# Kernel tuning notes

Measured on AMD Instinct MI355X. Metric: run time of the kernel, lower is better.

## Reference

```python
import jax, jax.numpy as jnp
import numpy as np

B, F, DIN, HID, H, E, NC = 2048, 32, 64, 128, 4, 262144, 10
N = B * F  # 65536 nodes


def setup_inputs() -> dict:
    key = jax.random.key(0)
    ks = jax.random.split(key, 20)
    p = lambda k, shape: jax.random.normal(k, shape, jnp.float32) * 0.05
    return {
        "emb": jax.random.normal(ks[0], (B, F, DIN), jnp.float32),
        "edge_index": jax.random.randint(ks[1], (2, E), 0, N, jnp.int32),
        "batch": (jnp.arange(N, dtype=jnp.int32) // F),
        # aligner Linear(64 -> 128)
        "W_align": p(ks[2], (DIN, HID)), "b_align": p(ks[3], (HID,)),
        # GATConv1: 128 -> 128, heads=4, concat
        "W1": p(ks[4], (HID, H * HID)),
        "att_src1": p(ks[5], (H, HID)), "att_dst1": p(ks[6], (H, HID)),
        "b1": p(ks[7], (H * HID,)),
        # GATConv2: 512 -> 128, heads=1, concat=False
        "W2": p(ks[8], (H * HID, HID)),
        "att_src2": p(ks[9], (1, HID)), "att_dst2": p(ks[10], (1, HID)),
        "b2": p(ks[11], (HID,)),
        # classifier MLP 128 -> 64 -> 10
        "Wc1": p(ks[12], (HID, HID // 2)), "bc1": p(ks[13], (HID // 2,)),
        "Wc2": p(ks[14], (HID // 2, NC)), "bc2": p(ks[15], (NC,)),
    }


def _gat(x, src, dst, W, a_src, a_dst, b, concat):
    # PyG GATConv (eval mode): per-edge additive attention + segment softmax over dst.
    n = x.shape[0]
    h, c = a_src.shape
    hx = (x @ W).reshape(n, h, c)                       # [N,H,C]
    al_s = jnp.einsum('nhc,hc->nh', hx, a_src)          # [N,H]
    al_d = jnp.einsum('nhc,hc->nh', hx, a_dst)
    e = jax.nn.leaky_relu(al_s[src] + al_d[dst], 0.2)   # [E,H]
    m = jax.ops.segment_max(e, dst, num_segments=n)
    m = jnp.where(jnp.isfinite(m), m, 0.0)
    ex = jnp.exp(e - m[dst])
    denom = jax.ops.segment_sum(ex, dst, num_segments=n)
    alpha = ex / (denom[dst] + 1e-16)                   # [E,H]
    out = jax.ops.segment_sum(alpha[:, :, None] * hx[src], dst, num_segments=n)
    out = out.reshape(n, h * c) if concat else out.mean(axis=1)
    return out + b


def reference(emb, edge_index, batch, W_align, b_align, W1, att_src1, att_dst1, b1,
              W2, att_src2, att_dst2, b2, Wc1, bc1, Wc2, bc2):
    # fused align: Linear over stacked field embeddings, then flatten to nodes
    x = (emb @ W_align + b_align).reshape(N, HID)
    # add self-loops (PyG GATConv default)
    loop = jnp.arange(N, dtype=edge_index.dtype)
    src = jnp.concatenate([edge_index[0], loop])
    dst = jnp.concatenate([edge_index[1], loop])
    x = _gat(x, src, dst, W1, att_src1, att_dst1, b1, concat=True)
    x = jax.nn.elu(x)
    x = _gat(x, src, dst, W2, att_src2, att_dst2, b2, concat=False)
    # global mean pool per graph
    g = jax.ops.segment_sum(x, batch, num_segments=B)
    cnt = jax.ops.segment_sum(jnp.ones((N, 1), x.dtype), batch, num_segments=B)
    g = g / jnp.maximum(cnt, 1.0)
    # classifier head (dropout off in eval)
    hcls = jax.nn.leaky_relu(g @ Wc1 + bc1, 0.01)
    return hcls @ Wc2 + bc2
```

## Files before the change

### kernel.cpp

```cpp
#include <hip/hip_runtime.h>


namespace {

constexpr int NNODE = 65536;
constexpr int NEDGE = 262144;
constexpr int NGRAPH = 2048;
constexpr int FPG = 32;

typedef __attribute__((ext_vector_type(8))) short bf16x8;
typedef __attribute__((ext_vector_type(4))) float f32x4;

__device__ __forceinline__ float lrelu02(float x) { return x > 0.f ? x : 0.2f * x; }
__device__ __forceinline__ float bf_lo(unsigned u) { return __uint_as_float(u << 16); }
__device__ __forceinline__ float bf_hi(unsigned u) { return __uint_as_float(u & 0xffff0000u); }
__device__ __forceinline__ float b2f(unsigned short u) { return __uint_as_float(((unsigned)u) << 16); }
__device__ __forceinline__ unsigned short f2b(float f) {
  unsigned u = __float_as_uint(f);
  return (unsigned short)((u + 0x7fffu + ((u >> 16) & 1u)) >> 16);
}

__device__ __forceinline__ void gload16(const void* g, unsigned short* l) {
  __builtin_amdgcn_global_load_lds((const __attribute__((address_space(1))) void*)g,
                                   (__attribute__((address_space(3))) void*)l, 16, 0, 0);
}


__global__ __launch_bounds__(256) void prep_kernel(const float* __restrict__ W1, const float* __restrict__ W2,
                                                   const float* __restrict__ Wa, const float* __restrict__ as1,
                                                   const float* __restrict__ ad1, unsigned short* __restrict__ w1t,
                                                   unsigned short* __restrict__ w2t, unsigned short* __restrict__ wat,
                                                   float* __restrict__ vs1, float* __restrict__ vd1,
                                                   int* __restrict__ deg) {
  int b = blockIdx.x;
  int tid = threadIdx.x;
  if (b < 256) {
    int idx = b * 256 + tid;
    int n = idx >> 7, k = idx & 127;
    w1t[idx] = f2b(W1[(size_t)k * 512 + n]);
  } else if (b < 512) {
    int idx = (b - 256) * 256 + tid;
    int n = idx >> 9, k = idx & 511;
    w2t[idx] = f2b(W2[(size_t)k * 128 + n]);
  } else if (b < 544) {
    int idx = (b - 512) * 256 + tid;
    int n = idx >> 6, k = idx & 63;
    wat[idx] = f2b(Wa[(size_t)k * 128 + n]);
  } else if (b < 546) {
    int idx = (b - 544) * 256 + tid;
    int h = idx >> 7, c = idx & 127;
    float s = 0.f, d = 0.f;
    const float* wrow = W1 + (size_t)c * 512 + h * 128;
    const float* ar = as1 + h * 128;
    const float* dr = ad1 + h * 128;
    for (int j = 0; j < 128; ++j) {
      float w = wrow[j];
      s += w * ar[j];
      d += w * dr[j];
    }
    vs1[idx] = s;
    vd1[idx] = d;
  } else {
    int idx = (b - 546) * 256 + tid;
    int4 z;
    z.x = 0; z.y = 0; z.z = 0; z.w = 0;
    *(int4*)&deg[idx * 4] = z;
  }
}


__global__ __launch_bounds__(256) void hist_kernel(const int* __restrict__ dst, int* __restrict__ deg) {
  int e = blockIdx.x * 256 + threadIdx.x;
  if (e < NEDGE) atomicAdd(&deg[dst[e]], 1);
}

__global__ __launch_bounds__(1024) void scan_kernel(const int* __restrict__ deg, int* __restrict__ rowptr,
                                                    int* __restrict__ cursor) {
  __shared__ int sums[1024];
  int t = threadIdx.x;
  int base = t * 64;
  int d[64];
  int s = 0;
#pragma unroll
  for (int i = 0; i < 16; ++i) {
    int4 v = *(const int4*)&deg[base + i * 4];
    d[4 * i] = v.x; d[4 * i + 1] = v.y; d[4 * i + 2] = v.z; d[4 * i + 3] = v.w;
    s += v.x + v.y + v.z + v.w;
  }
  sums[t] = s;
  __syncthreads();
  for (int off = 1; off < 1024; off <<= 1) {
    int v = (t >= off) ? sums[t - off] : 0;
    __syncthreads();
    sums[t] += v;
    __syncthreads();
  }
  int run = (t == 0) ? 0 : sums[t - 1];
#pragma unroll
  for (int i = 0; i < 16; ++i) {
    int4 r;
    r.x = run; run += d[4 * i];
    r.y = run; run += d[4 * i + 1];
    r.z = run; run += d[4 * i + 2];
    r.w = run; run += d[4 * i + 3];
    *(int4*)&rowptr[base + i * 4] = r;
    *(int4*)&cursor[base + i * 4] = r;
  }
  if (t == 1023) rowptr[NNODE] = run;
}

__global__ __launch_bounds__(256) void scatter_kernel(const int* __restrict__ src, const int* __restrict__ dst,
                                                      int* __restrict__ cursor, int* __restrict__ csr_src,
                                                      int* __restrict__ csr_dst) {
  int e = blockIdx.x * 256 + threadIdx.x;
  if (e < NEDGE) {
    int s = src[e], d = dst[e];
    int p = atomicAdd(&cursor[d], 1);
    csr_src[p] = s;
    csr_dst[p] = d;
  }
}


__global__ __launch_bounds__(256) void edgew1_kernel(const int* __restrict__ csr_src, const int* __restrict__ csr_dst,
                                                     const float* __restrict__ al_s, const float* __restrict__ al_d,
                                                     float* __restrict__ w1) {
  int p = blockIdx.x * 256 + threadIdx.x;
  if (p >= NEDGE) return;
  int s = csr_src[p], d = csr_dst[p];
  float4 as = *(const float4*)&al_s[s * 4];
  float4 ad = *(const float4*)&al_d[d * 4];
  float4 w;
  w.x = expf(lrelu02(as.x + ad.x));
  w.y = expf(lrelu02(as.y + ad.y));
  w.z = expf(lrelu02(as.z + ad.z));
  w.w = expf(lrelu02(as.w + ad.w));
  *(float4*)&w1[(size_t)p * 4] = w;
}

__global__ __launch_bounds__(256) void edgew2_kernel(const int* __restrict__ csr_src, const int* __restrict__ csr_dst,
                                                     const float* __restrict__ al_s, const float* __restrict__ al_d,
                                                     float* __restrict__ w2) {
  int p = blockIdx.x * 256 + threadIdx.x;
  if (p >= NEDGE) return;
  w2[p] = expf(lrelu02(al_s[csr_src[p]] + al_d[csr_dst[p]]));
}


__device__ __forceinline__ bf16x8 frag_ld(const unsigned short* lds, int row, int kbyte) {
  const char* base = (const char*)lds + row * 128;
  int sw = (row & 7) << 4;
  uint2 lo = *(const uint2*)(base + (kbyte ^ sw));
  uint2 hi = *(const uint2*)(base + ((kbyte + 32) ^ sw));
  union { bf16x8 v; uint2 u2[2]; } f;
  f.u2[0] = lo;
  f.u2[1] = hi;
  return f.v;
}

__device__ __forceinline__ bf16x8 frag_ld_x(const unsigned short* lds, int row, int kbyte) {
  const char* base = (const char*)lds + row * 256;
  int sw = (row & 7) << 4;
  uint2 lo = *(const uint2*)(base + (kbyte ^ sw));
  uint2 hi = *(const uint2*)(base + ((kbyte + 32) ^ sw));
  union { bf16x8 v; uint2 u2[2]; } f;
  f.u2[0] = lo;
  f.u2[1] = hi;
  return f.v;
}


__global__ __launch_bounds__(256) void align_mfma_kernel(const float* __restrict__ emb,
                                                         const unsigned short* __restrict__ wat,
                                                         const float* __restrict__ bias,
                                                         unsigned short* __restrict__ x0) {
  __shared__ char smem[36864];
  unsigned short* Ae = (unsigned short*)smem;
  unsigned short* Wt = (unsigned short*)(smem + 16384);
  const int tid = threadIdx.x;
  const int lane = tid & 63;
  const int w = tid >> 6;
  const size_t bm = (size_t)blockIdx.x * 128;
  const int ln = lane & 15, lg = lane >> 4;
  const int kb0 = lg << 3;

  {
    int r8 = lane >> 3;
    int b8 = (lane & 7) << 4;
#pragma unroll
    for (int i = 0; i < 4; ++i) {
      int row = w * 32 + i * 8 + r8;
      int bcol = b8 ^ ((row & 7) << 4);
      gload16((const char*)wat + row * 128 + bcol, Wt + w * 2048 + i * 512);
    }
  }
#pragma unroll
  for (int i = 0; i < 4; ++i) {
    int slot = i * 256 + tid;
    int row = slot >> 3;
    int c16 = slot & 7;
    const float* sp = emb + (bm + row) * 64 + c16 * 8;
    float4 a = *(const float4*)sp;
    float4 b = *(const float4*)(sp + 4);
    ushort4 o0, o1;
    o0.x = f2b(a.x); o0.y = f2b(a.y); o0.z = f2b(a.z); o0.w = f2b(a.w);
    o1.x = f2b(b.x); o1.y = f2b(b.y); o1.z = f2b(b.z); o1.w = f2b(b.w);
    char* dp = (char*)Ae + row * 128 + ((c16 * 16) ^ ((row & 7) << 4));
    *(ushort4*)dp = o0;
    *(ushort4*)(dp + 8) = o1;
  }
  __syncthreads();

  f32x4 zero = {0.f, 0.f, 0.f, 0.f};
  f32x4 acc[2][8];
#pragma unroll
  for (int i = 0; i < 2; ++i)
#pragma unroll
    for (int j = 0; j < 8; ++j) acc[i][j] = zero;

#pragma unroll
  for (int kw = 0; kw < 2; ++kw) {
    bf16x8 af0 = frag_ld(Ae, w * 32 + ln, kw * 64 + kb0);
    bf16x8 af1 = frag_ld(Ae, w * 32 + 16 + ln, kw * 64 + kb0);
#pragma unroll
    for (int nf = 0; nf < 8; ++nf) {
      bf16x8 bfr = frag_ld(Wt, nf * 16 + ln, kw * 64 + kb0);
      acc[0][nf] = __builtin_amdgcn_mfma_f32_16x16x32_bf16(af0, bfr, acc[0][nf], 0, 0, 0);
      acc[1][nf] = __builtin_amdgcn_mfma_f32_16x16x32_bf16(af1, bfr, acc[1][nf], 0, 0, 0);
    }
  }

  float bval[8];
#pragma unroll
  for (int nf = 0; nf < 8; ++nf) bval[nf] = bias[nf * 16 + ln];
  __syncthreads();
  unsigned short* Cs = (unsigned short*)smem;
#pragma unroll
  for (int mf = 0; mf < 2; ++mf) {
#pragma unroll
    for (int r = 0; r < 4; ++r) {
      unsigned short* rp = Cs + (w * 32 + mf * 16 + lg * 4 + r) * 136 + ln;
#pragma unroll
      for (int nf = 0; nf < 8; ++nf) rp[nf * 16] = f2b(acc[mf][nf][r] + bval[nf]);
    }
  }
  __syncthreads();
  const int r16 = tid >> 4;
  const int cchunk = (tid & 15) * 8;
#pragma unroll
  for (int it = 0; it < 8; ++it) {
    int row = it * 16 + r16;
    *(uint4*)(x0 + (bm + row) * 128 + cchunk) = *(const uint4*)(Cs + row * 136 + cchunk);
  }
}


__global__ __launch_bounds__(256, 2) void fused12_kernel(const unsigned short* __restrict__ ybar,
                                                         const unsigned short* __restrict__ w1t,
                                                         const unsigned short* __restrict__ w2t,
                                                         const float* __restrict__ b1,
                                                         unsigned short* __restrict__ hx2) {
  __shared__ char smem[65536];
  unsigned short* Ws = (unsigned short*)smem;
  unsigned short* Ys = Ws + 16384;

  const int tid = threadIdx.x;
  const int lane = tid & 63;
  const int w = tid >> 6;
  const size_t bm = (size_t)blockIdx.x * 128;

  const int ln = lane & 15, lg = lane >> 4;
  const int kb0 = lg << 3;
  const int drow = lane >> 4;
  const int dcol = (lane & 15) << 4;

  f32x4 zero = {0.f, 0.f, 0.f, 0.f};
  f32x4 acc2[2][8];
#pragma unroll
  for (int i = 0; i < 2; ++i)
#pragma unroll
    for (int j = 0; j < 8; ++j) acc2[i][j] = zero;

  for (int h = 0; h < 4; ++h) {
    if (h) __syncthreads();
#pragma unroll
    for (int i = 0; i < 8; ++i) {
      int row = w * 32 + i * 4 + drow;
      int bcol = dcol ^ ((row & 7) << 4);
      gload16((const char*)w1t + ((size_t)(h * 128 + row) << 8) + bcol, Ws + w * 4096 + i * 512);
      gload16((const char*)ybar + ((bm + row) << 10) + (h << 8) + bcol, Ys + w * 4096 + i * 512);
    }
    __syncthreads();

    f32x4 acc1[8][2];
#pragma unroll
    for (int i = 0; i < 8; ++i) {
      acc1[i][0] = zero;
      acc1[i][1] = zero;
    }
#pragma unroll
    for (int kw = 0; kw < 4; ++kw) {
      bf16x8 bfr0 = frag_ld_x(Ys, w * 32 + ln, kw * 64 + kb0);
      bf16x8 bfr1 = frag_ld_x(Ys, w * 32 + 16 + ln, kw * 64 + kb0);
#pragma unroll
      for (int ct = 0; ct < 8; ++ct) {
        bf16x8 af = frag_ld_x(Ws, ct * 16 + ln, kw * 64 + kb0);
        acc1[ct][0] = __builtin_amdgcn_mfma_f32_16x16x32_bf16(af, bfr0, acc1[ct][0], 0, 0, 0);
        acc1[ct][1] = __builtin_amdgcn_mfma_f32_16x16x32_bf16(af, bfr1, acc1[ct][1], 0, 0, 0);
      }
    }
    __syncthreads();

#pragma unroll
    for (int i = 0; i < 8; ++i) {
      int row = w * 32 + i * 4 + drow;
      int bcol = dcol ^ ((row & 7) << 4);
      gload16((const char*)w2t + ((size_t)row << 10) + (h << 8) + bcol, Ws + w * 4096 + i * 512);
    }
    __syncthreads();

#pragma unroll
    for (int kw = 0; kw < 4; ++kw) {
      float4 b_lo = *(const float4*)&b1[h * 128 + kw * 32 + lg * 4];
      float4 b_hi = *(const float4*)&b1[h * 128 + kw * 32 + 16 + lg * 4];
      bf16x8 af2[2];
#pragma unroll
      for (int mf = 0; mf < 2; ++mf) {
        union { bf16x8 v; unsigned short u[8]; } t;
#pragma unroll
        for (int r = 0; r < 4; ++r) {
          float vlo = acc1[2 * kw][mf][r] + ((const float*)&b_lo)[r];
          float vhi = acc1[2 * kw + 1][mf][r] + ((const float*)&b_hi)[r];
          vlo = vlo > 0.f ? vlo : __expf(vlo) - 1.f;
          vhi = vhi > 0.f ? vhi : __expf(vhi) - 1.f;
          t.u[r] = f2b(vlo);
          t.u[4 + r] = f2b(vhi);
        }
        af2[mf] = t.v;
      }
#pragma unroll
      for (int nf = 0; nf < 8; ++nf) {
        bf16x8 bfr = frag_ld_x(Ws, nf * 16 + ln, kw * 64 + kb0);
        acc2[0][nf] = __builtin_amdgcn_mfma_f32_16x16x32_bf16(af2[0], bfr, acc2[0][nf], 0, 0, 0);
        acc2[1][nf] = __builtin_amdgcn_mfma_f32_16x16x32_bf16(af2[1], bfr, acc2[1][nf], 0, 0, 0);
      }
    }
  }

  __syncthreads();
  unsigned short* Cs = (unsigned short*)smem;
#pragma unroll
  for (int mf = 0; mf < 2; ++mf) {
#pragma unroll
    for (int r = 0; r < 4; ++r) {
      unsigned short* rp = Cs + (w * 32 + mf * 16 + lg * 4 + r) * 136 + ln;
#pragma unroll
      for (int nf = 0; nf < 8; ++nf) rp[nf * 16] = f2b(acc2[mf][nf][r]);
    }
  }
  __syncthreads();
  const int r16 = tid >> 4;
  const int cchunk = (tid & 15) * 8;
#pragma unroll
  for (int it = 0; it < 8; ++it) {
    int row = it * 16 + r16;
    *(uint4*)(hx2 + (bm + row) * 128 + cchunk) = *(const uint4*)(Cs + row * 136 + cchunk);
  }
}


__global__ __launch_bounds__(256) void al1_kernel(const unsigned short* __restrict__ x0,
                                                  const float* __restrict__ vs1, const float* __restrict__ vd1,
                                                  float* __restrict__ al_s, float* __restrict__ al_d) {
  int n = blockIdx.x * 4 + (threadIdx.x >> 6);
  int lane = threadIdx.x & 63;
  unsigned v = *(const unsigned*)&x0[(size_t)n * 128 + lane * 2];
  float v0 = bf_lo(v), v1 = bf_hi(v);
  float r[8];
#pragma unroll
  for (int h = 0; h < 4; ++h) {
    float2 as = *(const float2*)&vs1[h * 128 + lane * 2];
    float2 ad = *(const float2*)&vd1[h * 128 + lane * 2];
    r[h] = v0 * as.x + v1 * as.y;
    r[4 + h] = v0 * ad.x + v1 * ad.y;
  }
#pragma unroll
  for (int off = 32; off; off >>= 1) {
#pragma unroll
    for (int j = 0; j < 8; ++j) r[j] += __shfl_xor(r[j], off);
  }
  if (lane < 4)
    al_s[n * 4 + lane] = r[lane];
  else if (lane < 8)
    al_d[n * 4 + lane - 4] = r[lane];
}

__global__ __launch_bounds__(256) void al2_kernel(const unsigned short* __restrict__ hx,
                                                  const float* __restrict__ att_src,
                                                  const float* __restrict__ att_dst,
                                                  float* __restrict__ al_s, float* __restrict__ al_d) {
  int n = blockIdx.x * 4 + (threadIdx.x >> 6);
  int lane = threadIdx.x & 63;
  unsigned v = *(const unsigned*)&hx[(size_t)n * 128 + lane * 2];
  float v0 = bf_lo(v), v1 = bf_hi(v);
  float2 as = *(const float2*)&att_src[lane * 2];
  float2 ad = *(const float2*)&att_dst[lane * 2];
  float s = v0 * as.x + v1 * as.y;
  float d = v0 * ad.x + v1 * ad.y;
  for (int off = 32; off; off >>= 1) {
    s += __shfl_down(s, off);
    d += __shfl_down(d, off);
  }
  if (lane == 0) {
    al_s[n] = s;
    al_d[n] = d;
  }
}


__global__ __launch_bounds__(256) void agg1_kernel(const unsigned short* __restrict__ x0,
                                                   const float* __restrict__ al_s, const float* __restrict__ al_d,
                                                   const int* __restrict__ rowptr, const int* __restrict__ csr_src,
                                                   const float* __restrict__ w1, unsigned short* __restrict__ ybar) {
  int n = blockIdx.x * 4 + (threadIdx.x >> 6);
  int c2 = (threadIdx.x & 63) * 2;
  float4 As4 = *(const float4*)&al_s[n * 4];
  float4 Ad4 = *(const float4*)&al_d[n * 4];
  float w00 = expf(lrelu02(As4.x + Ad4.x));
  float w01 = expf(lrelu02(As4.y + Ad4.y));
  float w02 = expf(lrelu02(As4.z + Ad4.z));
  float w03 = expf(lrelu02(As4.w + Ad4.w));
  unsigned u = *(const unsigned*)&x0[(size_t)n * 128 + c2];
  float lo = bf_lo(u), hi = bf_hi(u);
  float a00 = w00 * lo, a01 = w01 * lo, a02 = w02 * lo, a03 = w03 * lo;
  float a10 = w00 * hi, a11 = w01 * hi, a12 = w02 * hi, a13 = w03 * hi;
  float d0 = w00, d1 = w01, d2 = w02, d3 = w03;
  int p0 = rowptr[n], p1 = rowptr[n + 1];
  int p = p0;
  for (; p + 4 <= p1; p += 4) {
    int s0 = csr_src[p], s1 = csr_src[p + 1], s2 = csr_src[p + 2], s3 = csr_src[p + 3];
    float4 wA = *(const float4*)&w1[(size_t)p * 4];
    float4 wB = *(const float4*)&w1[(size_t)(p + 1) * 4];
    float4 wC = *(const float4*)&w1[(size_t)(p + 2) * 4];
    float4 wD = *(const float4*)&w1[(size_t)(p + 3) * 4];
    unsigned u0 = *(const unsigned*)&x0[(size_t)s0 * 128 + c2];
    unsigned u1 = *(const unsigned*)&x0[(size_t)s1 * 128 + c2];
    unsigned u2 = *(const unsigned*)&x0[(size_t)s2 * 128 + c2];
    unsigned u3 = *(const unsigned*)&x0[(size_t)s3 * 128 + c2];
    float l0 = bf_lo(u0), h0 = bf_hi(u0);
    float l1 = bf_lo(u1), h1 = bf_hi(u1);
    float l2 = bf_lo(u2), h2 = bf_hi(u2);
    float l3 = bf_lo(u3), h3 = bf_hi(u3);
    a00 += wA.x * l0 + wB.x * l1 + wC.x * l2 + wD.x * l3;
    a01 += wA.y * l0 + wB.y * l1 + wC.y * l2 + wD.y * l3;
    a02 += wA.z * l0 + wB.z * l1 + wC.z * l2 + wD.z * l3;
    a03 += wA.w * l0 + wB.w * l1 + wC.w * l2 + wD.w * l3;
    a10 += wA.x * h0 + wB.x * h1 + wC.x * h2 + wD.x * h3;
    a11 += wA.y * h0 + wB.y * h1 + wC.y * h2 + wD.y * h3;
    a12 += wA.z * h0 + wB.z * h1 + wC.z * h2 + wD.z * h3;
    a13 += wA.w * h0 + wB.w * h1 + wC.w * h2 + wD.w * h3;
    d0 += wA.x + wB.x + wC.x + wD.x;
    d1 += wA.y + wB.y + wC.y + wD.y;
    d2 += wA.z + wB.z + wC.z + wD.z;
    d3 += wA.w + wB.w + wC.w + wD.w;
  }
  for (; p < p1; ++p) {
    int s = csr_src[p];
    float4 wA = *(const float4*)&w1[(size_t)p * 4];
    unsigned uu = *(const unsigned*)&x0[(size_t)s * 128 + c2];
    float l = bf_lo(uu), hh = bf_hi(uu);
    a00 += wA.x * l; a01 += wA.y * l; a02 += wA.z * l; a03 += wA.w * l;
    a10 += wA.x * hh; a11 += wA.y * hh; a12 += wA.z * hh; a13 += wA.w * hh;
    d0 += wA.x; d1 += wA.y; d2 += wA.z; d3 += wA.w;
  }
  unsigned short* yb = ybar + (size_t)n * 512 + c2;
  float i0 = 1.f / (d0 + 1e-16f), i1 = 1.f / (d1 + 1e-16f);
  float i2 = 1.f / (d2 + 1e-16f), i3 = 1.f / (d3 + 1e-16f);
  ushort2 o;
  o.x = f2b(a00 * i0); o.y = f2b(a10 * i0); *(ushort2*)(yb + 0) = o;
  o.x = f2b(a01 * i1); o.y = f2b(a11 * i1); *(ushort2*)(yb + 128) = o;
  o.x = f2b(a02 * i2); o.y = f2b(a12 * i2); *(ushort2*)(yb + 256) = o;
  o.x = f2b(a03 * i3); o.y = f2b(a13 * i3); *(ushort2*)(yb + 384) = o;
}


__global__ __launch_bounds__(256) void agg2_kernel(const unsigned short* __restrict__ hx,
                                                   const float* __restrict__ al_s, const float* __restrict__ al_d,
                                                   const int* __restrict__ rowptr, const int* __restrict__ csr_src,
                                                   const float* __restrict__ w2, const float* __restrict__ b2,
                                                   unsigned short* __restrict__ out) {
  int n = blockIdx.x * 4 + (threadIdx.x >> 6);
  int c2 = (threadIdx.x & 63) * 2;
  float w0 = expf(lrelu02(al_s[n] + al_d[n]));
  unsigned u = *(const unsigned*)&hx[(size_t)n * 128 + c2];
  float acc0 = w0 * bf_lo(u), acc1 = w0 * bf_hi(u);
  float den = w0;
  int p0 = rowptr[n], p1 = rowptr[n + 1];
  int p = p0;
  for (; p + 4 <= p1; p += 4) {
    int s0 = csr_src[p], s1 = csr_src[p + 1], s2 = csr_src[p + 2], s3 = csr_src[p + 3];
    float wa = w2[p], wb = w2[p + 1], wc = w2[p + 2], wd = w2[p + 3];
    unsigned u0 = *(const unsigned*)&hx[(size_t)s0 * 128 + c2];
    unsigned u1 = *(const unsigned*)&hx[(size_t)s1 * 128 + c2];
    unsigned u2 = *(const unsigned*)&hx[(size_t)s2 * 128 + c2];
    unsigned u3 = *(const unsigned*)&hx[(size_t)s3 * 128 + c2];
    acc0 += wa * bf_lo(u0) + wb * bf_lo(u1) + wc * bf_lo(u2) + wd * bf_lo(u3);
    acc1 += wa * bf_hi(u0) + wb * bf_hi(u1) + wc * bf_hi(u2) + wd * bf_hi(u3);
    den += wa + wb + wc + wd;
  }
  for (; p < p1; ++p) {
    int s = csr_src[p];
    float w = w2[p];
    unsigned uu = *(const unsigned*)&hx[(size_t)s * 128 + c2];
    acc0 += w * bf_lo(uu);
    acc1 += w * bf_hi(uu);
    den += w;
  }
  float inv = 1.f / (den + 1e-16f);
  ushort2 o;
  o.x = f2b(acc0 * inv + b2[c2]);
  o.y = f2b(acc1 * inv + b2[c2 + 1]);
  *(ushort2*)&out[(size_t)n * 128 + c2] = o;
}


__global__ __launch_bounds__(128) void poolcls_kernel(const unsigned short* __restrict__ x,
                                                      const float* __restrict__ Wc1, const float* __restrict__ bc1,
                                                      const float* __restrict__ Wc2, const float* __restrict__ bc2,
                                                      float* __restrict__ out) {
  __shared__ float g[128];
  __shared__ float hcls[64];
  int b = blockIdx.x;
  int t = threadIdx.x;
  const unsigned short* base = x + (size_t)b * FPG * 128;
  float s = 0.f;
#pragma unroll
  for (int i = 0; i < FPG; ++i) s += b2f(base[i * 128 + t]);
  g[t] = s * (1.0f / FPG);
  __syncthreads();
  if (t < 64) {
    float a = bc1[t];
#pragma unroll 4
    for (int k = 0; k < 128; ++k) a += g[k] * Wc1[k * 64 + t];
    hcls[t] = a > 0.f ? a : 0.01f * a;
  }
  __syncthreads();
  if (t < 10) {
    float a = bc2[t];
#pragma unroll
    for (int k = 0; k < 64; ++k) a += hcls[k] * Wc2[k * 10 + t];
    out[b * 10 + t] = a;
  }
}

}

extern "C" void kernel_launch(void* const* d_in, const int* in_sizes, int n_in,
                              void* d_out, int out_size, void* d_ws, size_t ws_size,
                              hipStream_t stream) {
  const float* emb = (const float*)d_in[0];
  const int* edge = (const int*)d_in[1];
  const float* W_align = (const float*)d_in[3];
  const float* b_align = (const float*)d_in[4];
  const float* W1 = (const float*)d_in[5];
  const float* att_src1 = (const float*)d_in[6];
  const float* att_dst1 = (const float*)d_in[7];
  const float* b1 = (const float*)d_in[8];
  const float* W2 = (const float*)d_in[9];
  const float* att_src2 = (const float*)d_in[10];
  const float* att_dst2 = (const float*)d_in[11];
  const float* b2 = (const float*)d_in[12];
  const float* Wc1 = (const float*)d_in[13];
  const float* bc1 = (const float*)d_in[14];
  const float* Wc2 = (const float*)d_in[15];
  const float* bc2 = (const float*)d_in[16];

  char* ws = (char*)d_ws;
  size_t off = 0;
  auto alloc = [&](size_t bytes) -> char* {
    char* p = ws + off;
    off += (bytes + 255) & ~(size_t)255;
    return p;
  };
  unsigned short* x0 = (unsigned short*)alloc((size_t)NNODE * 128 * 2);
  unsigned short* ybar = (unsigned short*)alloc((size_t)NNODE * 512 * 2);
  unsigned short* hx2 = (unsigned short*)alloc((size_t)NNODE * 128 * 2);
  unsigned short* out2 = (unsigned short*)alloc((size_t)NNODE * 128 * 2);
  float* al_s1 = (float*)alloc((size_t)NNODE * 4 * 4);
  float* al_d1 = (float*)alloc((size_t)NNODE * 4 * 4);
  float* al_s2 = (float*)alloc((size_t)NNODE * 4);
  float* al_d2 = (float*)alloc((size_t)NNODE * 4);
  int* deg = (int*)alloc((size_t)NNODE * 4);
  int* rowptr = (int*)alloc((size_t)(NNODE + 1) * 4);
  int* cursor = (int*)alloc((size_t)NNODE * 4);
  int* csr_src = (int*)alloc((size_t)NEDGE * 4);
  int* csr_dst = (int*)alloc((size_t)NEDGE * 4);
  float* w1 = (float*)alloc((size_t)NEDGE * 4 * 4);
  float* w2 = (float*)alloc((size_t)NEDGE * 4);
  unsigned short* w1t = (unsigned short*)alloc((size_t)512 * 128 * 2);
  unsigned short* w2t = (unsigned short*)alloc((size_t)128 * 512 * 2);
  unsigned short* wat = (unsigned short*)alloc((size_t)128 * 64 * 2);
  float* vs1 = (float*)alloc((size_t)512 * 4);
  float* vd1 = (float*)alloc((size_t)512 * 4);

  const int* src = edge;
  const int* dst = edge + NEDGE;

  prep_kernel<<<610, 256, 0, stream>>>(W1, W2, W_align, att_src1, att_dst1,
                                       w1t, w2t, wat, vs1, vd1, deg);
  hist_kernel<<<NEDGE / 256, 256, 0, stream>>>(dst, deg);
  scan_kernel<<<1, 1024, 0, stream>>>(deg, rowptr, cursor);
  scatter_kernel<<<NEDGE / 256, 256, 0, stream>>>(src, dst, cursor, csr_src, csr_dst);

  align_mfma_kernel<<<512, 256, 0, stream>>>(emb, wat, b_align, x0);
  al1_kernel<<<NNODE / 4, 256, 0, stream>>>(x0, vs1, vd1, al_s1, al_d1);
  edgew1_kernel<<<NEDGE / 256, 256, 0, stream>>>(csr_src, csr_dst, al_s1, al_d1, w1);
  agg1_kernel<<<NNODE / 4, 256, 0, stream>>>(x0, al_s1, al_d1, rowptr, csr_src, w1, ybar);
  fused12_kernel<<<512, 256, 0, stream>>>(ybar, w1t, w2t, b1, hx2);
  al2_kernel<<<NNODE / 4, 256, 0, stream>>>(hx2, att_src2, att_dst2, al_s2, al_d2);
  edgew2_kernel<<<NEDGE / 256, 256, 0, stream>>>(csr_src, csr_dst, al_s2, al_d2, w2);
  agg2_kernel<<<NNODE / 4, 256, 0, stream>>>(hx2, al_s2, al_d2, rowptr, csr_src, w2, b2, out2);
  poolcls_kernel<<<NGRAPH, 128, 0, stream>>>(out2, Wc1, bc1, Wc2, bc2, (float*)d_out);
}
```

Measured before the change: 234.9 us.

## Load GAT weights directly from global and fuse layer-2 attention logits

The fused GEMM kernel no longer stages W1/W2 tiles in LDS. It reads weight fragments straight from global memory (relying on L2/cache) and keeps only a per-wave ybar tile in LDS, which removes most block-wide barriers and cuts shared memory to about 34KB, allowing more blocks per CU. The layer-2 attention dot products (al_s2/al_d2) are computed from the output tile already in LDS, so the separate al2 kernel launch and its re-read of hx2 are gone. The trade-off is uncoalesced, repeated global weight loads inside the MFMA loops, plus a serial 128-element dot product done by half the threads.

New measurement: 315.9 us. 1.34x slower.

```diff
diff --git a/kernel.cpp b/kernel.cpp
--- a/kernel.cpp
+++ b/kernel.cpp
@@ -158,14 +158,19 @@
   return f.v;
 }
 
-__device__ __forceinline__ bf16x8 frag_ld_x(const unsigned short* lds, int row, int kbyte) {
-  const char* base = (const char*)lds + row * 256;
+__device__ __forceinline__ bf16x8 ys_frag(const char* base, int row, int kbyte) {
+  const char* rb = base + row * 256;
   int sw = (row & 7) << 4;
-  uint2 lo = *(const uint2*)(base + (kbyte ^ sw));
-  uint2 hi = *(const uint2*)(base + ((kbyte + 32) ^ sw));
   union { bf16x8 v; uint2 u2[2]; } f;
-  f.u2[0] = lo;
-  f.u2[1] = hi;
+  f.u2[0] = *(const uint2*)(rb + (kbyte ^ sw));
+  f.u2[1] = *(const uint2*)(rb + ((kbyte + 32) ^ sw));
+  return f.v;
+}
+
+__device__ __forceinline__ bf16x8 gfrag(const unsigned short* p) {
+  union { bf16x8 v; uint2 u2[2]; } f;
+  f.u2[0] = *(const uint2*)p;
+  f.u2[1] = *(const uint2*)(p + 16);
   return f.v;
 }
 
@@ -259,20 +264,20 @@
                                                          const unsigned short* __restrict__ w1t,
                                                          const unsigned short* __restrict__ w2t,
                                                          const float* __restrict__ b1,
-                                                         unsigned short* __restrict__ hx2) {
-  __shared__ char smem[65536];
-  unsigned short* Ws = (unsigned short*)smem;
-  unsigned short* Ys = Ws + 16384;
-
+                                                         const float* __restrict__ as2,
+                                                         const float* __restrict__ ad2,
+                                                         unsigned short* __restrict__ hx2,
+                                                         float* __restrict__ al_s2, float* __restrict__ al_d2) {
+  __shared__ char smem[34816];
   const int tid = threadIdx.x;
   const int lane = tid & 63;
   const int w = tid >> 6;
   const size_t bm = (size_t)blockIdx.x * 128;
-
   const int ln = lane & 15, lg = lane >> 4;
-  const int kb0 = lg << 3;
-  const int drow = lane >> 4;
-  const int dcol = (lane & 15) << 4;
+  char* ybase = smem + w * 8192;
+
+  const int srow4 = lane >> 4;
+  const int scol = (lane & 15) << 4;
 
   f32x4 zero = {0.f, 0.f, 0.f, 0.f};
   f32x4 acc2[2][8];
@@ -282,15 +287,17 @@
     for (int j = 0; j < 8; ++j) acc2[i][j] = zero;
 
   for (int h = 0; h < 4; ++h) {
-    if (h) __syncthreads();
+    uint4 yv[8];
 #pragma unroll
     for (int i = 0; i < 8; ++i) {
-      int row = w * 32 + i * 4 + drow;
-      int bcol = dcol ^ ((row & 7) << 4);
-      gload16((const char*)w1t + ((size_t)(h * 128 + row) << 8) + bcol, Ws + w * 4096 + i * 512);
-      gload16((const char*)ybar + ((bm + row) << 10) + (h << 8) + bcol, Ys + w * 4096 + i * 512);
-    }
-    __syncthreads();
+      int lr = i * 4 + srow4;
+      yv[i] = *(const uint4*)((const char*)ybar + (bm + w * 32 + lr) * 1024 + h * 256 + scol);
+    }
+#pragma unroll
+    for (int i = 0; i < 8; ++i) {
+      int lr = i * 4 + srow4;
+      *(uint4*)(ybase + lr * 256 + (scol ^ ((lr & 7) << 4))) = yv[i];
+    }
 
     f32x4 acc1[8][2];
 #pragma unroll
@@ -300,24 +307,16 @@
     }
 #pragma unroll
     for (int kw = 0; kw < 4; ++kw) {
-      bf16x8 bfr0 = frag_ld_x(Ys, w * 32 + ln, kw * 64 + kb0);
-      bf16x8 bfr1 = frag_ld_x(Ys, w * 32 + 16 + ln, kw * 64 + kb0);
+      int kb = kw * 64 + (lg << 3);
+      bf16x8 bfr0 = ys_frag(ybase, ln, kb);
+      bf16x8 bfr1 = ys_frag(ybase, 16 + ln, kb);
 #pragma unroll
       for (int ct = 0; ct < 8; ++ct) {
-        bf16x8 af = frag_ld_x(Ws, ct * 16 + ln, kw * 64 + kb0);
+        bf16x8 af = gfrag(w1t + (((h * 128) + ct * 16 + ln) << 7) + kw * 32 + (lg << 2));
         acc1[ct][0] = __builtin_amdgcn_mfma_f32_16x16x32_bf16(af, bfr0, acc1[ct][0], 0, 0, 0);
         acc1[ct][1] = __builtin_amdgcn_mfma_f32_16x16x32_bf16(af, bfr1, acc1[ct][1], 0, 0, 0);
       }
     }
-    __syncthreads();
-
-#pragma unroll
-    for (int i = 0; i < 8; ++i) {
-      int row = w * 32 + i * 4 + drow;
-      int bcol = dcol ^ ((row & 7) << 4);
-      gload16((const char*)w2t + ((size_t)row << 10) + (h << 8) + bcol, Ws + w * 4096 + i * 512);
-    }
-    __syncthreads();
 
 #pragma unroll
     for (int kw = 0; kw < 4; ++kw) {
@@ -340,7 +339,7 @@
       }
 #pragma unroll
       for (int nf = 0; nf < 8; ++nf) {
-        bf16x8 bfr = frag_ld_x(Ws, nf * 16 + ln, kw * 64 + kb0);
+        bf16x8 bfr = gfrag(w2t + ((nf * 16 + ln) << 9) + h * 128 + kw * 32 + (lg << 2));
         acc2[0][nf] = __builtin_amdgcn_mfma_f32_16x16x32_bf16(af2[0], bfr, acc2[0][nf], 0, 0, 0);
         acc2[1][nf] = __builtin_amdgcn_mfma_f32_16x16x32_bf16(af2[1], bfr, acc2[1][nf], 0, 0, 0);
       }
@@ -359,6 +358,18 @@
     }
   }
   __syncthreads();
+  if (tid < 128) {
+    const unsigned short* row = Cs + tid * 136;
+    float s = 0.f, d = 0.f;
+#pragma unroll 4
+    for (int c = 0; c < 128; ++c) {
+      float v = b2f(row[c]);
+      s += v * as2[c];
+      d += v * ad2[c];
+    }
+    al_s2[bm + tid] = s;
+    al_d2[bm + tid] = d;
+  }
   const int r16 = tid >> 4;
   const int cchunk = (tid & 15) * 8;
 #pragma unroll
@@ -393,28 +404,6 @@
     al_s[n * 4 + lane] = r[lane];
   else if (lane < 8)
     al_d[n * 4 + lane - 4] = r[lane];
-}
-
-__global__ __launch_bounds__(256) void al2_kernel(const unsigned short* __restrict__ hx,
-                                                  const float* __restrict__ att_src,
-                                                  const float* __restrict__ att_dst,
-                                                  float* __restrict__ al_s, float* __restrict__ al_d) {
-  int n = blockIdx.x * 4 + (threadIdx.x >> 6);
-  int lane = threadIdx.x & 63;
-  unsigned v = *(const unsigned*)&hx[(size_t)n * 128 + lane * 2];
-  float v0 = bf_lo(v), v1 = bf_hi(v);
-  float2 as = *(const float2*)&att_src[lane * 2];
-  float2 ad = *(const float2*)&att_dst[lane * 2];
-  float s = v0 * as.x + v1 * as.y;
-  float d = v0 * ad.x + v1 * ad.y;
-  for (int off = 32; off; off >>= 1) {
-    s += __shfl_down(s, off);
-    d += __shfl_down(d, off);
-  }
-  if (lane == 0) {
-    al_s[n] = s;
-    al_d[n] = d;
-  }
 }
 
 
@@ -616,8 +605,7 @@
   al1_kernel<<<NNODE / 4, 256, 0, stream>>>(x0, vs1, vd1, al_s1, al_d1);
   edgew1_kernel<<<NEDGE / 256, 256, 0, stream>>>(csr_src, csr_dst, al_s1, al_d1, w1);
   agg1_kernel<<<NNODE / 4, 256, 0, stream>>>(x0, al_s1, al_d1, rowptr, csr_src, w1, ybar);
-  fused12_kernel<<<512, 256, 0, stream>>>(ybar, w1t, w2t, b1, hx2);
-  al2_kernel<<<NNODE / 4, 256, 0, stream>>>(hx2, att_src2, att_dst2, al_s2, al_d2);
+  fused12_kernel<<<512, 256, 0, stream>>>(ybar, w1t, w2t, b1, att_src2, att_dst2, hx2, al_s2, al_d2);
   edgew2_kernel<<<NEDGE / 256, 256, 0, stream>>>(csr_src, csr_dst, al_s2, al_d2, w2);
   agg2_kernel<<<NNODE / 4, 256, 0, stream>>>(hx2, al_s2, al_d2, rowptr, csr_src, w2, b2, out2);
   poolcls_kernel<<<NGRAPH, 128, 0, stream>>>(out2, Wc1, bc1, Wc2, bc2, (float*)d_out);
```
